# Performance work log

Measured on AMD Instinct MI355X. Metric: run time of the kernel, lower is better.

## Reference

```python
import jax, jax.numpy as jnp
import numpy as np
from jax import lax

B, C, H, W = 64, 3, 256, 256
E, D = 64, 32          # expert_nums, embed_dim
TOP_K = 2
NOISE_EPS = 0.01
ALPHA = 0.8


def setup_inputs() -> dict:
    key = jax.random.key(0)
    ks = jax.random.split(key, 16)
    n = lambda k, shape, s=0.05: jax.random.normal(k, shape, jnp.float32) * s
    return {
        "task_id": jax.random.randint(ks[0], (B,), 0, 10),
        "degradation_info": jax.random.normal(ks[1], (B, C, H, W), jnp.float32),
        "noise": jax.random.normal(ks[2], (B, E), jnp.float32),
        "mlp_w1": n(ks[3], (1, D)), "mlp_b1": jnp.zeros((D,), jnp.float32),
        "mlp_w2": n(ks[4], (D, D)), "mlp_b2": jnp.zeros((D,), jnp.float32),
        "conv1_w": n(ks[5], (16, C, 3, 3)), "conv1_b": jnp.zeros((16,), jnp.float32),
        "conv2_w": n(ks[6], (32, 16, 3, 3)), "conv2_b": jnp.zeros((32,), jnp.float32),
        "deg_w": n(ks[7], (32, D)), "deg_b": jnp.zeros((D,), jnp.float32),
        "expert_keys": jax.random.normal(ks[8], (E, D), jnp.float32),
        "gate_w": n(ks[9], (E, E)), "gate_b": jnp.zeros((E,), jnp.float32),
        "noise_w": n(ks[10], (E, E)), "noise_b": jnp.zeros((E,), jnp.float32),
    }


def _conv(x, w):
    return lax.conv_general_dilated(
        x, w, window_strides=(1, 1), padding="SAME",
        dimension_numbers=("NCHW", "OIHW", "NCHW"))


def reference(task_id, degradation_info, noise,
              mlp_w1, mlp_b1, mlp_w2, mlp_b2,
              conv1_w, conv1_b, conv2_w, conv2_b,
              deg_w, deg_b, expert_keys,
              gate_w, gate_b, noise_w, noise_b):
    # task embedding: Linear(1,D) -> ReLU -> Linear(D,D)
    t = task_id.astype(jnp.float32)[:, None]                       # [B,1]
    task_embed = jax.nn.relu(t @ mlp_w1 + mlp_b1) @ mlp_w2 + mlp_b2  # [B,D]

    # degradation conv embed: conv->relu->conv->relu->global avg pool
    h = jax.nn.relu(_conv(degradation_info, conv1_w) + conv1_b[None, :, None, None])
    h = jax.nn.relu(_conv(h, conv2_w) + conv2_b[None, :, None, None])
    feat = h.mean(axis=(2, 3))                                     # [B,32]
    deg_embed = feat @ deg_w + deg_b                               # [B,D]

    combined = task_embed + (1.0 - ALPHA) * deg_embed              # [B,D]
    sim = combined @ expert_keys.T / jnp.sqrt(jnp.float32(D))      # [B,E]
    expert_weight = jax.nn.softmax(sim, axis=1)

    clean_logits = expert_weight @ gate_w + gate_b                 # [B,E]
    stddev = jax.nn.softplus(expert_weight @ noise_w + noise_b) + NOISE_EPS
    logits = clean_logits + noise * stddev                         # train=True path

    top_logits, top_idx = lax.top_k(logits, min(TOP_K + 1, E))
    tk_logits = top_logits[:, :TOP_K]                              # [B,k]
    tk_idx = top_idx[:, :TOP_K]
    tk_gates = jax.nn.softmax(tk_logits, axis=1)

    rows = jnp.arange(logits.shape[0])[:, None]
    gates = jnp.zeros_like(logits).at[rows, tk_idx].set(tk_gates)  # scatter
    load = gates.sum(axis=0)                                       # [E]
    return gates, load
```

## Files before the change

### kernel.cpp

```cpp
#include <hip/hip_runtime.h>
#include <math.h>

typedef __attribute__((ext_vector_type(8)))  short  short8;
typedef __attribute__((ext_vector_type(4)))  float  floatx4;
typedef __attribute__((ext_vector_type(16))) float  floatx16;
typedef __attribute__((ext_vector_type(2)))  float  floatx2;
typedef __attribute__((ext_vector_type(2)))  unsigned uintx2;

__device__ __forceinline__ short bf16rne(float f) {
    unsigned u = __float_as_uint(f);
    unsigned r = (u + 0x7FFFu + ((u >> 16) & 1u)) >> 16;
    return (short)r;
}

__device__ __forceinline__ unsigned pk2(float a, float b) {
#if __has_builtin(__builtin_amdgcn_cvt_pk_bf16_f32)
    auto t = __builtin_amdgcn_cvt_pk_bf16_f32(a, b);
    unsigned u; __builtin_memcpy(&u, &t, 4); return u;
#else
    return (unsigned)(unsigned short)bf16rne(a) |
           ((unsigned)(unsigned short)bf16rne(b) << 16);
#endif
}

#define WS_FRAG_OFF  8192
#define WS_BIAS1_OFF (WS_FRAG_OFF + 10 * 64 * 16)
#define WS_BIAS2_OFF (WS_BIAS1_OFF + 64 * 16)

__global__ __launch_bounds__(256) void build_frags_kernel(
    const float* __restrict__ w1,
    const float* __restrict__ b1,
    const float* __restrict__ w2,
    const float* __restrict__ b2,
    void* __restrict__ ws,
    float* __restrict__ out)
{
    const int t = threadIdx.x;
    float* feat = (float*)ws;
    for (int i = t; i < 2048; i += 256) feat[i] = 0.0f;
    if (t >= 64 && t < 128) out[4096 + (t - 64)] = 0.0f;

    if (t < 64) {
        const int lane = t;
        const int q = lane >> 4, ml = lane & 15;
        const int n32 = lane & 31, half = lane >> 5;
        short8* F = (short8*)((char*)ws + WS_FRAG_OFF);

        short8 W1;
#pragma unroll
        for (int j = 0; j < 8; ++j) {
            int k = q * 8 + j;
            W1[j] = (k < 27) ? bf16rne(w1[ml * 27 + k]) : (short)0;
        }
        F[lane] = W1;

#pragma unroll
        for (int s = 0; s < 9; ++s) {
            short8 Bs;
#pragma unroll
            for (int j = 0; j < 8; ++j) {
                int ic = half * 8 + j;
                Bs[j] = bf16rne(w2[(n32 * 16 + ic) * 9 + s]);
            }
            F[(1 + s) * 64 + lane] = Bs;
        }
        floatx4 bv;
#pragma unroll
        for (int r = 0; r < 4; ++r) bv[r] = b1[q * 4 + r];
        ((floatx4*)((char*)ws + WS_BIAS1_OFF))[lane] = bv;
        ((float*)((char*)ws + WS_BIAS2_OFF))[lane] = b2[n32];
    }
}

__device__ __forceinline__ void conv1_tile(
    short* __restrict__ s_h1, const short* __restrict__ s_in,
    const int* lcS, int gOff, int wIdx, bool valid, bool q3,
    short8 W1, floatx4 biasv)
{
    short8 Bx;
#pragma unroll
    for (int j = 0; j < 8; ++j) Bx[j] = s_in[gOff + lcS[j]];
    if (q3) { Bx[3] = 0; Bx[4] = 0; Bx[5] = 0; Bx[6] = 0; Bx[7] = 0; }
    floatx4 acc = biasv;
    acc = __builtin_amdgcn_mfma_f32_16x16x32_bf16(W1, Bx, acc, 0, 0, 0);
    float v0 = fmaxf(acc[0], 0.f), v1 = fmaxf(acc[1], 0.f);
    float v2 = fmaxf(acc[2], 0.f), v3 = fmaxf(acc[3], 0.f);
    if (!valid) { v0 = 0.f; v1 = 0.f; v2 = 0.f; v3 = 0.f; }
    uintx2 w; w.x = pk2(v0, v1); w.y = pk2(v2, v3);
    *(uintx2*)&s_h1[wIdx] = w;
}

__global__ __launch_bounds__(256, 6) void conv_feat_kernel(
    const float* __restrict__ x,
    const void*  __restrict__ ws_ro,
    float* __restrict__ feat_sum)
{
    __shared__ short s_in[3 * 20 * 24];
    __shared__ short s_h1[324 * 24];
    __shared__ float s_part[4][32];

    const int t    = threadIdx.x;
    const int lane = t & 63, wv = t >> 6;
    const int q    = lane >> 4, ml = lane & 15;
    const int n32  = lane & 31, half = lane >> 5;
    const int tx = blockIdx.x, ty = blockIdx.y, b = blockIdx.z;
    const bool border = (tx == 0) | (tx == 15) | (ty == 0) | (ty == 15);

    const short8* F = (const short8*)((const char*)ws_ro + WS_FRAG_OFF);
    short8 W1 = F[lane];
    short8 B2[9];
#pragma unroll
    for (int s = 0; s < 9; ++s) B2[s] = F[(1 + s) * 64 + lane];
    floatx4 biasv = ((const floatx4*)((const char*)ws_ro + WS_BIAS1_OFF))[lane];
    float   b2v   = ((const float*)((const char*)ws_ro + WS_BIAS2_OFF))[lane];

    int lcS[8];
#pragma unroll
    for (int j = 0; j < 8; ++j) {
        int k = q * 8 + j;
        int kk = (k < 27) ? k : 0;
        int c = kk / 9, s = kk % 9;
        lcS[j] = (c * 20 + s / 3) * 24 + (s % 3);
    }
    const bool q3 = (q == 3);
    const int swz1 = (q * 4) ^ ((ml & 1) * 8);

    const int gy0 = ty * 16 - 2, gx0 = tx * 16 - 2;
    const float* xb = x + (size_t)b * 3 * 65536;
    if (!border) {
        for (int i = t; i < 600; i += 256) {
            int c = i / 200, rem = i % 200, r = rem / 10, c2 = rem % 10;
            const float* p = xb + c * 65536 + (gy0 + r) * 256 + gx0 + 2 * c2;
            floatx2 v = *(const floatx2*)p;
            *(unsigned*)&s_in[(c * 20 + r) * 24 + 2 * c2] = pk2(v.x, v.y);
        }
    } else {
        for (int i = t; i < 600; i += 256) {
            int c = i / 200, rem = i % 200, r = rem / 10, c2 = rem % 10;
            int gy = gy0 + r, gx = gx0 + 2 * c2;
            float v0 = 0.0f, v1 = 0.0f;
            if ((unsigned)gy < 256u) {
                const float* p = xb + c * 65536 + gy * 256;
                if ((unsigned)gx < 256u)       v0 = p[gx];
                if ((unsigned)(gx + 1) < 256u) v1 = p[gx + 1];
            }
            *(unsigned*)&s_in[(c * 20 + r) * 24 + 2 * c2] = pk2(v0, v1);
        }
    }
    __syncthreads();

    if (!border) {
#pragma unroll
        for (int i = 0; i < 4; ++i) {
            int tile = wv + 4 * i;
            conv1_tile(s_h1, s_in, lcS, ml + tile * 24,
                       (tile * 18 + ml) * 24 + swz1, true, q3, W1, biasv);
        }
        int t4 = wv + 16;
        if (wv < 2) {
            conv1_tile(s_h1, s_in, lcS, ml + t4 * 24,
                       (t4 * 18 + ml) * 24 + swz1, true, q3, W1, biasv);
        } else {
            int cc = wv - 2;
            conv1_tile(s_h1, s_in, lcS, ml * 24 + 16 + cc,
                       (ml * 18 + 16 + cc) * 24 + ((q * 4) ^ (cc * 8)),
                       true, q3, W1, biasv);
        }
        if (wv == 0) {
            int ml2 = ml & 3;
            int iy = 16 + (ml2 >> 1), ix = 16 + (ml2 & 1);
            conv1_tile(s_h1, s_in, lcS, iy * 24 + ix,
                       (iy * 18 + ix) * 24 + ((q * 4) ^ ((ml2 & 1) * 8)),
                       true, q3, W1, biasv);
        }
    } else {
        const bool gxOK = (unsigned)(tx * 16 - 1 + ml) < 256u;
#pragma unroll
        for (int i = 0; i < 4; ++i) {
            int tile = wv + 4 * i;
            bool rowOK = (unsigned)(ty * 16 - 1 + tile) < 256u;
            conv1_tile(s_h1, s_in, lcS, ml + tile * 24,
                       (tile * 18 + ml) * 24 + swz1, rowOK & gxOK, q3, W1, biasv);
        }
        int t4 = wv + 16;
        if (wv < 2) {
            bool rowOK = (unsigned)(ty * 16 - 1 + t4) < 256u;
            conv1_tile(s_h1, s_in, lcS, ml + t4 * 24,
                       (t4 * 18 + ml) * 24 + swz1, rowOK & gxOK, q3, W1, biasv);
        } else {
            int cc = wv - 2;
            bool ok = ((unsigned)(ty * 16 - 1 + ml) < 256u) &
                      ((unsigned)(tx * 16 + 15 + cc) < 256u);
            conv1_tile(s_h1, s_in, lcS, ml * 24 + 16 + cc,
                       (ml * 18 + 16 + cc) * 24 + ((q * 4) ^ (cc * 8)),
                       ok, q3, W1, biasv);
        }
        if (wv == 0) {
            int ml2 = ml & 3;
            int iy = 16 + (ml2 >> 1), ix = 16 + (ml2 & 1);
            bool ok = ((unsigned)(ty * 16 - 1 + iy) < 256u) &
                      ((unsigned)(tx * 16 - 1 + ix) < 256u);
            conv1_tile(s_h1, s_in, lcS, iy * 24 + ix,
                       (iy * 18 + ix) * 24 + ((q * 4) ^ ((ml2 & 1) * 8)),
                       ok, q3, W1, biasv);
        }
    }
    __syncthreads();

    float part = 0.0f;
    const int prow0 = (n32 >> 4), pcol = n32 & 15;
    const int sw  = (half * 8) ^ ((n32 & 1) * 8);
    const int swX = sw ^ 8;
#pragma unroll
    for (int tt = 0; tt < 2; ++tt) {
        int pix0 = (2 * (2 * wv + tt) + prow0) * 18 + pcol;
        const short* A0 = s_h1 + pix0 * 24 + sw;
        const short* A1 = s_h1 + pix0 * 24 + swX;
        floatx16 acc;
#pragma unroll
        for (int r = 0; r < 16; ++r) acc[r] = b2v;
#pragma unroll
        for (int s = 0; s < 9; ++s) {
            const int ky = s / 3, kx = s % 3;
            const short* p = ((kx & 1) ? A1 : A0) + (ky * 18 + kx) * 24;
            short8 Ax = *(const short8*)p;
            acc = __builtin_amdgcn_mfma_f32_32x32x16_bf16(Ax, B2[s], acc, 0, 0, 0);
        }
#pragma unroll
        for (int r = 0; r < 16; ++r) part += fmaxf(acc[r], 0.0f);
    }
    part += __shfl_xor(part, 32);
    if (lane < 32) s_part[wv][n32] = part;
    __syncthreads();
    if (t < 32) {
        float ssum = s_part[0][t] + s_part[1][t] + s_part[2][t] + s_part[3][t];
        atomicAdd(feat_sum + b * 32 + t, ssum);
    }
}

__global__ __launch_bounds__(64) void router_gate_kernel(
    const int* __restrict__ task_id,
    const float* __restrict__ noise,
    const float* __restrict__ mlp_w1,
    const float* __restrict__ mlp_b1,
    const float* __restrict__ mlp_w2,
    const float* __restrict__ mlp_b2,
    const float* __restrict__ deg_w,
    const float* __restrict__ deg_b,
    const float* __restrict__ keys,
    const float* __restrict__ gate_w,
    const float* __restrict__ gate_b,
    const float* __restrict__ noise_w,
    const float* __restrict__ noise_b,
    const float* __restrict__ feat_sum,
    float* __restrict__ out)
{
    const int b = blockIdx.x;
    const int e = threadIdx.x;

    __shared__ float s_te[32];
    __shared__ float s_comb[32];
    __shared__ float s_ew[64];

    if (e < 32) {
        float tf = (float)task_id[b];
        s_te[e] = fmaxf(tf * mlp_w1[e] + mlp_b1[e], 0.0f);
    }
    __syncthreads();
    if (e < 32) {
        float acc = mlp_b2[e];
        for (int k = 0; k < 32; ++k) acc += s_te[k] * mlp_w2[k * 32 + e];
        float dacc = deg_b[e];
        for (int c = 0; c < 32; ++c)
            dacc += (feat_sum[b * 32 + c] * (1.0f / 65536.0f)) * deg_w[c * 32 + e];
        s_comb[e] = acc + 0.2f * dacc;
    }
    __syncthreads();

    float s = 0.0f;
    for (int d = 0; d < 32; ++d) s += s_comb[d] * keys[e * 32 + d];
    s *= 0.17677669529663687f;

    float m = s;
    for (int off = 32; off; off >>= 1) m = fmaxf(m, __shfl_xor(m, off));
    float p = expf(s - m);
    float sum = p;
    for (int off = 32; off; off >>= 1) sum += __shfl_xor(sum, off);
    float w = p / sum;
    s_ew[e] = w;
    __syncthreads();

    float cl = gate_b[e], nz = noise_b[e];
    for (int k = 0; k < 64; ++k) {
        float ewk = s_ew[k];
        cl += ewk * gate_w[k * 64 + e];
        nz += ewk * noise_w[k * 64 + e];
    }
    float sp = (nz > 20.0f) ? nz : log1pf(expf(nz));
    float logit = cl + noise[b * 64 + e] * (sp + 0.01f);

    float v0 = logit; int i0 = e;
    for (int off = 32; off; off >>= 1) {
        float ov = __shfl_xor(v0, off);
        int   oi = __shfl_xor(i0, off);
        if (ov > v0 || (ov == v0 && oi < i0)) { v0 = ov; i0 = oi; }
    }
    float v1 = (e == i0) ? -INFINITY : logit; int i1 = e;
    for (int off = 32; off; off >>= 1) {
        float ov = __shfl_xor(v1, off);
        int   oi = __shfl_xor(i1, off);
        if (ov > v1 || (ov == v1 && oi < i1)) { v1 = ov; i1 = oi; }
    }

    float e1 = expf(v1 - v0);
    float g0 = 1.0f / (1.0f + e1);
    float g1 = e1 / (1.0f + e1);

    float g = (e == i0) ? g0 : (e == i1) ? g1 : 0.0f;
    out[b * 64 + e] = g;
    if (g != 0.0f) atomicAdd(out + 64 * 64 + e, g);
}

extern "C" void kernel_launch(void* const* d_in, const int* in_sizes, int n_in,
                              void* d_out, int out_size, void* d_ws, size_t ws_size,
                              hipStream_t stream) {
    const int*   task_id = (const int*)d_in[0];
    const float* x       = (const float*)d_in[1];
    const float* noise   = (const float*)d_in[2];
    const float* mlp_w1  = (const float*)d_in[3];
    const float* mlp_b1  = (const float*)d_in[4];
    const float* mlp_w2  = (const float*)d_in[5];
    const float* mlp_b2  = (const float*)d_in[6];
    const float* conv1_w = (const float*)d_in[7];
    const float* conv1_b = (const float*)d_in[8];
    const float* conv2_w = (const float*)d_in[9];
    const float* conv2_b = (const float*)d_in[10];
    const float* deg_w   = (const float*)d_in[11];
    const float* deg_b   = (const float*)d_in[12];
    const float* keys    = (const float*)d_in[13];
    const float* gate_w  = (const float*)d_in[14];
    const float* gate_b  = (const float*)d_in[15];
    const float* noise_w = (const float*)d_in[16];
    const float* noise_b = (const float*)d_in[17];

    float* out  = (float*)d_out;
    float* feat = (float*)d_ws;

    build_frags_kernel<<<1, 256, 0, stream>>>(conv1_w, conv1_b, conv2_w,
                                              conv2_b, d_ws, out);
    dim3 gridA(16, 16, 64);
    conv_feat_kernel<<<gridA, 256, 0, stream>>>(x, d_ws, feat);
    router_gate_kernel<<<64, 64, 0, stream>>>(
        task_id, noise, mlp_w1, mlp_b1, mlp_w2, mlp_b2, deg_w, deg_b, keys,
        gate_w, gate_b, noise_w, noise_b, feat, out);
}
```

Baseline: 199.0 us.

## Store conv1 input pixel-interleaved and gather im2col with vector LDS loads

The staged input tile becomes pixel-major with the three channels plus a zero pad packed into 8 bytes. Each conv1 MFMA operand is then built from three 64-bit LDS loads instead of eight scalar gathers. The reduction is split into two MFMAs: one covers positions 0-7 across channels, and a second covers position 8 with a separate weight fragment. The XOR swizzle on s_h1 is dropped, so conv2 reads are unswizzled. The goal is to cut LDS instruction count and address arithmetic, at the cost of an extra MFMA per tile and possible bank conflicts without the swizzle.

```diff
diff --git a/kernel.cpp b/kernel.cpp
--- a/kernel.cpp
+++ b/kernel.cpp
@@ -2,9 +2,9 @@
 #include <math.h>
 
 typedef __attribute__((ext_vector_type(8)))  short  short8;
+typedef __attribute__((ext_vector_type(4)))  short  svec4;
 typedef __attribute__((ext_vector_type(4)))  float  floatx4;
 typedef __attribute__((ext_vector_type(16))) float  floatx16;
-typedef __attribute__((ext_vector_type(2)))  float  floatx2;
 typedef __attribute__((ext_vector_type(2)))  unsigned uintx2;
 
 __device__ __forceinline__ short bf16rne(float f) {
@@ -12,7 +12,6 @@
     unsigned r = (u + 0x7FFFu + ((u >> 16) & 1u)) >> 16;
     return (short)r;
 }
-
 __device__ __forceinline__ unsigned pk2(float a, float b) {
 #if __has_builtin(__builtin_amdgcn_cvt_pk_bf16_f32)
     auto t = __builtin_amdgcn_cvt_pk_bf16_f32(a, b);
@@ -24,7 +23,7 @@
 }
 
 #define WS_FRAG_OFF  8192
-#define WS_BIAS1_OFF (WS_FRAG_OFF + 10 * 64 * 16)
+#define WS_BIAS1_OFF (WS_FRAG_OFF + 11 * 64 * 16)
 #define WS_BIAS2_OFF (WS_BIAS1_OFF + 64 * 16)
 
 __global__ __launch_bounds__(256) void build_frags_kernel(
@@ -46,13 +45,21 @@
         const int n32 = lane & 31, half = lane >> 5;
         short8* F = (short8*)((char*)ws + WS_FRAG_OFF);
 
-        short8 W1;
+        short8 W1a;
 #pragma unroll
         for (int j = 0; j < 8; ++j) {
-            int k = q * 8 + j;
-            W1[j] = (k < 27) ? bf16rne(w1[ml * 27 + k]) : (short)0;
-        }
-        F[lane] = W1;
+            int p = q * 2 + (j >> 2), c = j & 3;
+            W1a[j] = (c < 3) ? bf16rne(w1[ml * 27 + c * 9 + p]) : (short)0;
+        }
+        F[0 * 64 + lane] = W1a;
+
+        short8 W1b;
+#pragma unroll
+        for (int j = 0; j < 8; ++j) {
+            W1b[j] = (q == 0 && j < 3) ? bf16rne(w1[ml * 27 + j * 9 + 8])
+                                       : (short)0;
+        }
+        F[1 * 64 + lane] = W1b;
 
 #pragma unroll
         for (int s = 0; s < 9; ++s) {
@@ -62,7 +69,7 @@
                 int ic = half * 8 + j;
                 Bs[j] = bf16rne(w2[(n32 * 16 + ic) * 9 + s]);
             }
-            F[(1 + s) * 64 + lane] = Bs;
+            F[(2 + s) * 64 + lane] = Bs;
         }
         floatx4 bv;
 #pragma unroll
@@ -73,21 +80,29 @@
 }
 
 __device__ __forceinline__ void conv1_tile(
-    short* __restrict__ s_h1, const short* __restrict__ s_in,
-    const int* lcS, int gOff, int wIdx, bool valid, bool q3,
-    short8 W1, floatx4 biasv)
+    short* __restrict__ s_h1, const short* __restrict__ s_in4,
+    const int* lcB, int basePixByte, int wIdx, bool valid, bool wmask,
+    short8 W1a, short8 W1b, floatx4 biasv)
 {
-    short8 Bx;
-#pragma unroll
-    for (int j = 0; j < 8; ++j) Bx[j] = s_in[gOff + lcS[j]];
-    if (q3) { Bx[3] = 0; Bx[4] = 0; Bx[5] = 0; Bx[6] = 0; Bx[7] = 0; }
+    const char* base = (const char*)s_in4 + basePixByte;
+    svec4 r0 = *(const svec4*)(base + lcB[0]);
+    svec4 r1 = *(const svec4*)(base + lcB[1]);
+    svec4 r2 = *(const svec4*)(base + lcB[2]);
+    short8 Bx, By;
+    Bx[0]=r0[0]; Bx[1]=r0[1]; Bx[2]=r0[2]; Bx[3]=r0[3];
+    Bx[4]=r1[0]; Bx[5]=r1[1]; Bx[6]=r1[2]; Bx[7]=r1[3];
+    By[0]=r2[0]; By[1]=r2[1]; By[2]=r2[2]; By[3]=r2[3];
+    By[4]=r2[0]; By[5]=r2[1]; By[6]=r2[2]; By[7]=r2[3];
     floatx4 acc = biasv;
-    acc = __builtin_amdgcn_mfma_f32_16x16x32_bf16(W1, Bx, acc, 0, 0, 0);
+    acc = __builtin_amdgcn_mfma_f32_16x16x32_bf16(W1a, Bx, acc, 0, 0, 0);
+    acc = __builtin_amdgcn_mfma_f32_16x16x32_bf16(W1b, By, acc, 0, 0, 0);
     float v0 = fmaxf(acc[0], 0.f), v1 = fmaxf(acc[1], 0.f);
     float v2 = fmaxf(acc[2], 0.f), v3 = fmaxf(acc[3], 0.f);
     if (!valid) { v0 = 0.f; v1 = 0.f; v2 = 0.f; v3 = 0.f; }
-    uintx2 w; w.x = pk2(v0, v1); w.y = pk2(v2, v3);
-    *(uintx2*)&s_h1[wIdx] = w;
+    if (wmask) {
+        uintx2 w; w.x = pk2(v0, v1); w.y = pk2(v2, v3);
+        *(uintx2*)&s_h1[wIdx] = w;
+    }
 }
 
 __global__ __launch_bounds__(256, 6) void conv_feat_kernel(
@@ -95,7 +110,7 @@
     const void*  __restrict__ ws_ro,
     float* __restrict__ feat_sum)
 {
-    __shared__ short s_in[3 * 20 * 24];
+    __shared__ short s_in4[20 * 20 * 4];
     __shared__ short s_h1[324 * 24];
     __shared__ float s_part[4][32];
 
@@ -107,123 +122,120 @@
     const bool border = (tx == 0) | (tx == 15) | (ty == 0) | (ty == 15);
 
     const short8* F = (const short8*)((const char*)ws_ro + WS_FRAG_OFF);
-    short8 W1 = F[lane];
+    short8 W1a = F[0 * 64 + lane];
+    short8 W1b = F[1 * 64 + lane];
     short8 B2[9];
 #pragma unroll
-    for (int s = 0; s < 9; ++s) B2[s] = F[(1 + s) * 64 + lane];
+    for (int s = 0; s < 9; ++s) B2[s] = F[(2 + s) * 64 + lane];
     floatx4 biasv = ((const floatx4*)((const char*)ws_ro + WS_BIAS1_OFF))[lane];
     float   b2v   = ((const float*)((const char*)ws_ro + WS_BIAS2_OFF))[lane];
 
-    int lcS[8];
-#pragma unroll
-    for (int j = 0; j < 8; ++j) {
-        int k = q * 8 + j;
-        int kk = (k < 27) ? k : 0;
-        int c = kk / 9, s = kk % 9;
-        lcS[j] = (c * 20 + s / 3) * 24 + (s % 3);
-    }
-    const bool q3 = (q == 3);
-    const int swz1 = (q * 4) ^ ((ml & 1) * 8);
+    int lcB[3];
+    {
+        int p0 = q * 2, p1 = q * 2 + 1;
+        lcB[0] = ((p0 / 3) * 20 + p0 % 3) * 8;
+        lcB[1] = ((p1 / 3) * 20 + p1 % 3) * 8;
+        lcB[2] = (2 * 20 + 2) * 8;
+    }
 
     const int gy0 = ty * 16 - 2, gx0 = tx * 16 - 2;
     const float* xb = x + (size_t)b * 3 * 65536;
     if (!border) {
-        for (int i = t; i < 600; i += 256) {
-            int c = i / 200, rem = i % 200, r = rem / 10, c2 = rem % 10;
-            const float* p = xb + c * 65536 + (gy0 + r) * 256 + gx0 + 2 * c2;
-            floatx2 v = *(const floatx2*)p;
-            *(unsigned*)&s_in[(c * 20 + r) * 24 + 2 * c2] = pk2(v.x, v.y);
+        for (int i = t; i < 400; i += 256) {
+            int r = i / 20, col = i % 20;
+            const float* p = xb + (gy0 + r) * 256 + (gx0 + col);
+            float v0 = p[0], v1 = p[65536], v2 = p[131072];
+            uintx2 w; w.x = pk2(v0, v1); w.y = pk2(v2, 0.f);
+            *(uintx2*)&s_in4[i * 4] = w;
         }
     } else {
-        for (int i = t; i < 600; i += 256) {
-            int c = i / 200, rem = i % 200, r = rem / 10, c2 = rem % 10;
-            int gy = gy0 + r, gx = gx0 + 2 * c2;
-            float v0 = 0.0f, v1 = 0.0f;
-            if ((unsigned)gy < 256u) {
-                const float* p = xb + c * 65536 + gy * 256;
-                if ((unsigned)gx < 256u)       v0 = p[gx];
-                if ((unsigned)(gx + 1) < 256u) v1 = p[gx + 1];
+        for (int i = t; i < 400; i += 256) {
+            int r = i / 20, col = i % 20;
+            int gy = gy0 + r, gx = gx0 + col;
+            float v0 = 0.f, v1 = 0.f, v2 = 0.f;
+            if ((unsigned)gy < 256u && (unsigned)gx < 256u) {
+                const float* p = xb + gy * 256 + gx;
+                v0 = p[0]; v1 = p[65536]; v2 = p[131072];
             }
-            *(unsigned*)&s_in[(c * 20 + r) * 24 + 2 * c2] = pk2(v0, v1);
-        }
-    }
-    __syncthreads();
-
+            uintx2 w; w.x = pk2(v0, v1); w.y = pk2(v2, 0.f);
+            *(uintx2*)&s_in4[i * 4] = w;
+        }
+    }
+    __syncthreads();
+
+    const int mlb = ml * 8;
+    const int wbase = ml * 24 + q * 4;
     if (!border) {
 #pragma unroll
         for (int i = 0; i < 4; ++i) {
             int tile = wv + 4 * i;
-            conv1_tile(s_h1, s_in, lcS, ml + tile * 24,
-                       (tile * 18 + ml) * 24 + swz1, true, q3, W1, biasv);
-        }
-        int t4 = wv + 16;
+            conv1_tile(s_h1, s_in4, lcB, tile * 160 + mlb,
+                       tile * 432 + wbase, true, true, W1a, W1b, biasv);
+        }
         if (wv < 2) {
-            conv1_tile(s_h1, s_in, lcS, ml + t4 * 24,
-                       (t4 * 18 + ml) * 24 + swz1, true, q3, W1, biasv);
+            int tile = wv + 16;
+            conv1_tile(s_h1, s_in4, lcB, tile * 160 + mlb,
+                       tile * 432 + wbase, true, true, W1a, W1b, biasv);
         } else {
             int cc = wv - 2;
-            conv1_tile(s_h1, s_in, lcS, ml * 24 + 16 + cc,
-                       (ml * 18 + 16 + cc) * 24 + ((q * 4) ^ (cc * 8)),
-                       true, q3, W1, biasv);
+            conv1_tile(s_h1, s_in4, lcB, ml * 160 + (16 + cc) * 8,
+                       (ml * 18 + 16 + cc) * 24 + q * 4, true, true,
+                       W1a, W1b, biasv);
         }
         if (wv == 0) {
             int ml2 = ml & 3;
             int iy = 16 + (ml2 >> 1), ix = 16 + (ml2 & 1);
-            conv1_tile(s_h1, s_in, lcS, iy * 24 + ix,
-                       (iy * 18 + ix) * 24 + ((q * 4) ^ ((ml2 & 1) * 8)),
-                       true, q3, W1, biasv);
+            conv1_tile(s_h1, s_in4, lcB, iy * 160 + ix * 8,
+                       (iy * 18 + ix) * 24 + q * 4, true, ml < 4,
+                       W1a, W1b, biasv);
         }
     } else {
         const bool gxOK = (unsigned)(tx * 16 - 1 + ml) < 256u;
 #pragma unroll
         for (int i = 0; i < 4; ++i) {
             int tile = wv + 4 * i;
-            bool rowOK = (unsigned)(ty * 16 - 1 + tile) < 256u;
-            conv1_tile(s_h1, s_in, lcS, ml + tile * 24,
-                       (tile * 18 + ml) * 24 + swz1, rowOK & gxOK, q3, W1, biasv);
-        }
-        int t4 = wv + 16;
+            bool ok = ((unsigned)(ty * 16 - 1 + tile) < 256u) & gxOK;
+            conv1_tile(s_h1, s_in4, lcB, tile * 160 + mlb,
+                       tile * 432 + wbase, ok, true, W1a, W1b, biasv);
+        }
         if (wv < 2) {
-            bool rowOK = (unsigned)(ty * 16 - 1 + t4) < 256u;
-            conv1_tile(s_h1, s_in, lcS, ml + t4 * 24,
-                       (t4 * 18 + ml) * 24 + swz1, rowOK & gxOK, q3, W1, biasv);
+            int tile = wv + 16;
+            bool ok = ((unsigned)(ty * 16 - 1 + tile) < 256u) & gxOK;
+            conv1_tile(s_h1, s_in4, lcB, tile * 160 + mlb,
+                       tile * 432 + wbase, ok, true, W1a, W1b, biasv);
         } else {
             int cc = wv - 2;
             bool ok = ((unsigned)(ty * 16 - 1 + ml) < 256u) &
                       ((unsigned)(tx * 16 + 15 + cc) < 256u);
-            conv1_tile(s_h1, s_in, lcS, ml * 24 + 16 + cc,
-                       (ml * 18 + 16 + cc) * 24 + ((q * 4) ^ (cc * 8)),
-                       ok, q3, W1, biasv);
+            conv1_tile(s_h1, s_in4, lcB, ml * 160 + (16 + cc) * 8,
+                       (ml * 18 + 16 + cc) * 24 + q * 4, ok, true,
+                       W1a, W1b, biasv);
         }
         if (wv == 0) {
             int ml2 = ml & 3;
             int iy = 16 + (ml2 >> 1), ix = 16 + (ml2 & 1);
             bool ok = ((unsigned)(ty * 16 - 1 + iy) < 256u) &
                       ((unsigned)(tx * 16 - 1 + ix) < 256u);
-            conv1_tile(s_h1, s_in, lcS, iy * 24 + ix,
-                       (iy * 18 + ix) * 24 + ((q * 4) ^ ((ml2 & 1) * 8)),
-                       ok, q3, W1, biasv);
+            conv1_tile(s_h1, s_in4, lcB, iy * 160 + ix * 8,
+                       (iy * 18 + ix) * 24 + q * 4, ok, ml < 4,
+                       W1a, W1b, biasv);
         }
     }
     __syncthreads();
 
     float part = 0.0f;
     const int prow0 = (n32 >> 4), pcol = n32 & 15;
-    const int sw  = (half * 8) ^ ((n32 & 1) * 8);
-    const int swX = sw ^ 8;
 #pragma unroll
     for (int tt = 0; tt < 2; ++tt) {
         int pix0 = (2 * (2 * wv + tt) + prow0) * 18 + pcol;
-        const short* A0 = s_h1 + pix0 * 24 + sw;
-        const short* A1 = s_h1 + pix0 * 24 + swX;
+        const short* A0 = s_h1 + pix0 * 24 + half * 8;
         floatx16 acc;
 #pragma unroll
         for (int r = 0; r < 16; ++r) acc[r] = b2v;
 #pragma unroll
         for (int s = 0; s < 9; ++s) {
             const int ky = s / 3, kx = s % 3;
-            const short* p = ((kx & 1) ? A1 : A0) + (ky * 18 + kx) * 24;
-            short8 Ax = *(const short8*)p;
+            short8 Ax = *(const short8*)(A0 + (ky * 18 + kx) * 24);
             acc = __builtin_amdgcn_mfma_f32_32x32x16_bf16(Ax, B2[s], acc, 0, 0, 0);
         }
 #pragma unroll
```

Measured after the change: 182.7 us. -8.2%, faster.
